# Optimization experiments

Measured on AMD Instinct MI355X. Metric: run time of the kernel, lower is better.

## Reference

```python
import jax, jax.numpy as jnp
import numpy as np

N, B, L = 1000, 16, 12
H, IN_DIM, OUT_DIM, E = 64, 3, 1, 16000


def _gru_cell(x, h, Wi, Wh, bi, bh):
    # torch nn.GRU gate order: r, z, n
    gi = x @ Wi.T + bi
    gh = h @ Wh.T + bh
    ir, iz, inn = jnp.split(gi, 3, axis=-1)
    hr, hz, hn = jnp.split(gh, 3, axis=-1)
    r = jax.nn.sigmoid(ir + hr)
    z = jax.nn.sigmoid(iz + hz)
    n = jnp.tanh(inn + r * hn)
    return (1.0 - z) * n + z * h


def setup_inputs():
    key = jax.random.key(0)
    ks = jax.random.split(key, 24)
    def rn(k, shape, s=0.1):
        return jax.random.normal(k, shape, dtype=jnp.float32) * s
    return {
        "hidden0": rn(ks[0], (N, B, H), 1.0),
        "hidden1": rn(ks[1], (N, B, H), 1.0),
        "features": rn(ks[2], (N, H), 1.0),
        "labels": rn(ks[3], (N, B, L, IN_DIM), 1.0),
        "edge_index": jax.random.randint(ks[4], (2, E), 0, N),
        # GRU1: input_dim -> H
        "Wi1": rn(ks[5], (3 * H, IN_DIM)), "Wh1": rn(ks[6], (3 * H, H)),
        "bi1": rn(ks[7], (3 * H,)), "bh1": rn(ks[8], (3 * H,)),
        # MetaGAT MLP: 2H -> 16 -> 2 -> 2H*H
        "W1": rn(ks[9], (16, 2 * H)), "b1": rn(ks[10], (16,)),
        "W2": rn(ks[11], (2, 16)), "b2": rn(ks[12], (2,)),
        "W3": rn(ks[13], (2 * H * H, 2)), "b3": rn(ks[14], (2 * H * H,)),
        # GRU2: H -> H
        "Wi2": rn(ks[15], (3 * H, H)), "Wh2": rn(ks[16], (3 * H, H)),
        "bi2": rn(ks[17], (3 * H,)), "bh2": rn(ks[18], (3 * H,)),
        # output layer: 2H -> OUT_DIM
        "Wo": rn(ks[19], (OUT_DIM, 2 * H)), "bo": rn(ks[20], (OUT_DIM,)),
    }


def reference(hidden0, hidden1, features, labels, edge_index,
              Wi1, Wh1, bi1, bh1, W1, b1, W2, b2, W3, b3,
              Wi2, Wh2, bi2, bh2, Wo, bo):
    n, b, length, _ = labels.shape
    h = Wh1.shape[1]
    out_dim = Wo.shape[0]
    in_dim = Wi1.shape[1]
    aux = labels[..., out_dim:]  # [N,B,L,aux_dim]
    # add self loops (as in MetaGAT.forward)
    loops = jnp.arange(n)
    src = jnp.concatenate([edge_index[0], loops])  # j, source
    dst = jnp.concatenate([edge_index[1], loops])  # i, target
    # per-edge weight matrices; features are constant across timesteps so hoist
    ft = jnp.concatenate([features[dst], features[src]], axis=-1)  # [Etot,2H]
    w = jax.nn.sigmoid(ft @ W1.T + b1)
    w = jax.nn.sigmoid(w @ W2.T + b2)
    w = (w @ W3.T + b3).reshape(-1, 2 * h, h)  # [Etot,2H,H]
    feat_b = jnp.broadcast_to(features[:, None, :], (n, b, features.shape[-1]))

    def step(carry, idx):
        h0, h1, prev = carry
        aux_prev = jnp.take(aux, jnp.maximum(idx - 1, 0), axis=2)  # [N,B,aux]
        # eval path (train_mode=False): feed back previous prediction
        data = jnp.where(idx == 0,
                         jnp.zeros((n, b, in_dim), labels.dtype),
                         jnp.concatenate([prev, aux_prev], axis=-1))
        h0n = _gru_cell(data.reshape(n * b, in_dim), h0.reshape(n * b, h),
                        Wi1, Wh1, bi1, bh1).reshape(n, b, h)
        # MetaGAT message passing
        st_j = h0n[src]                                  # [Etot,B,H]
        st = jnp.concatenate([h0n[dst], st_j], axis=-1)  # [Etot,B,2H]
        alpha = jax.nn.leaky_relu(jnp.einsum('ebk,ekh->ebh', st, w), 0.01)
        alpha = jax.nn.softmax(alpha, axis=1)            # softmax over batch dim (faithful to source)
        agg = jax.ops.segment_sum(alpha * st_j, dst, num_segments=n)
        gat = jax.nn.relu(agg)                           # [N,B,H]
        h1n = _gru_cell(gat.reshape(n * b, h), h1.reshape(n * b, h),
                        Wi2, Wh2, bi2, bh2).reshape(n, b, h)
        pred = jnp.concatenate([h1n, feat_b], axis=-1) @ Wo.T + bo  # [N,B,out_dim]
        return (h0n, h1n, pred), pred

    init = (hidden0, hidden1, jnp.zeros((n, b, out_dim), labels.dtype))
    _, preds = jax.lax.scan(step, init, jnp.arange(length))
    return jnp.moveaxis(preds, 0, 2)  # [N,B,L,out_dim]
```

## Files before the change

kernel.cpp:

```cpp
#include <hip/hip_runtime.h>

#define N_NODES 1000
#define BATCH 16
#define SEQ 12
#define IN_DIM 3
#define HDIM 64
#define E_EDGES 16000
#define EN (E_EDGES + N_NODES)
#define NB (N_NODES * BATCH)

typedef unsigned int u32;
typedef unsigned short u16;
typedef __fp16 h2_t __attribute__((ext_vector_type(2)));
typedef float f2_t __attribute__((ext_vector_type(2)));

__device__ __forceinline__ float sigmoidf(float x) { return 1.0f / (1.0f + expf(-x)); }

__device__ __forceinline__ u16 f2bf(float x) {
    u32 u = __builtin_bit_cast(u32, x);
    u32 r = (u + 0x7fffu + ((u >> 16) & 1u)) >> 16;
    return (u16)r;
}
__device__ __forceinline__ float bf2f(u32 h) {
    return __builtin_bit_cast(float, (h & 0xffffu) << 16);
}
__device__ __forceinline__ u32 pack2(float a, float b) {
    return (u32)f2bf(a) | ((u32)f2bf(b) << 16);
}

__device__ __forceinline__ u32 pkh2(float a, float b) {
    h2_t h = __builtin_amdgcn_cvt_pkrtz(a, b);
    return __builtin_bit_cast(u32, h);
}
#if __has_builtin(__builtin_amdgcn_fdot2)
__device__ __forceinline__ float dot2(u32 a, u32 b, float c) {
    return __builtin_amdgcn_fdot2(__builtin_bit_cast(h2_t, a),
                                  __builtin_bit_cast(h2_t, b), c, false);
}
#else
__device__ __forceinline__ float dot2(u32 a, u32 b, float c) {
    h2_t x = __builtin_bit_cast(h2_t, a);
    h2_t y = __builtin_bit_cast(h2_t, b);
    return c + (float)x.x * (float)y.x + (float)x.y * (float)y.y;
}
#endif

#if __has_builtin(__builtin_amdgcn_cvt_pk_f32_fp8)
__device__ __forceinline__ f2_t pkf8lo(u32 v) { return __builtin_amdgcn_cvt_pk_f32_fp8(v, false); }
__device__ __forceinline__ f2_t pkf8hi(u32 v) { return __builtin_amdgcn_cvt_pk_f32_fp8(v, true); }
#else
__device__ __forceinline__ f2_t pkf8lo(u32 v) {
    f2_t r; r.x = __builtin_amdgcn_cvt_f32_fp8(v, 0); r.y = __builtin_amdgcn_cvt_f32_fp8(v, 1); return r;
}
__device__ __forceinline__ f2_t pkf8hi(u32 v) {
    f2_t r; r.x = __builtin_amdgcn_cvt_f32_fp8(v, 2); r.y = __builtin_amdgcn_cvt_f32_fp8(v, 3); return r;
}
#endif

__global__ void prep_kernel(const float* __restrict__ hidden0,
                            const float* __restrict__ hidden1,
                            const float* __restrict__ features,
                            const float* __restrict__ W3,
                            const float* __restrict__ b3,
                            const float* __restrict__ Wo,
                            const float* __restrict__ bo,
                            const float* __restrict__ Wh1,
                            const float* __restrict__ Wi1,
                            const float* __restrict__ Wi2,
                            const float* __restrict__ Wh2,
                            float* __restrict__ h0, float* __restrict__ h1,
                            float* __restrict__ M,
                            float* __restrict__ Wh1T, float* __restrict__ Wi1T,
                            u32* __restrict__ W2H2,
                            float* __restrict__ fpred, float* __restrict__ prev)
{
    int tid = blockIdx.x * blockDim.x + threadIdx.x;
    int stride = gridDim.x * blockDim.x;

    for (int i = tid; i < NB * HDIM; i += stride) { h0[i] = hidden0[i]; h1[i] = hidden1[i]; }

    for (int i = tid; i < 64 * 384; i += stride) {
        int k = i / 384, c = i % 384;
        int grp = c / 64, h = c % 64;
        int kk = (grp < 3 ? k : 64 + k) * 64 + h;
        float val;
        if (grp == 0 || grp == 3)      val = W3[kk * 2 + 0];
        else if (grp == 1 || grp == 4) val = W3[kk * 2 + 1];
        else                           val = b3[kk];
        M[i] = val;
    }

    for (int i = tid; i < 192 * 64; i += stride) {
        int k = i / 192, gj = i % 192;
        Wh1T[i] = Wh1[gj * 64 + k];
    }
    for (int i = tid; i < 3 * 192; i += stride) {
        int c = i / 192, gj = i % 192;
        Wi1T[i] = Wi1[gj * 3 + c];
    }

    for (int i = tid; i < 32 * 384; i += stride) {
        int k2 = i / 384, cc = i % 384;
        float v0, v1;
        if (cc < 192) {
            v0 = Wi2[cc * 64 + 2 * k2]; v1 = Wi2[cc * 64 + 2 * k2 + 1];
        } else {
            int gj = cc - 192;
            v0 = Wh2[gj * 64 + 2 * k2]; v1 = Wh2[gj * 64 + 2 * k2 + 1];
        }
        W2H2[i] = pkh2(v0, v1);
    }

    for (int i = tid; i < NB; i += stride) prev[i] = 0.0f;

    for (int n = tid; n < N_NODES; n += stride) {
        float acc = bo[0];
        for (int h = 0; h < HDIM; ++h) acc += features[n * HDIM + h] * Wo[64 + h];
        fpred[n] = acc;
    }
}

__global__ void deg_init_kernel(int* __restrict__ deg)
{
    int n = blockIdx.x * blockDim.x + threadIdx.x;
    if (n < N_NODES) deg[n] = 1;
}

__global__ void deg_count_kernel(const int* __restrict__ edge_index, int* __restrict__ deg)
{
    int e = blockIdx.x * blockDim.x + threadIdx.x;
    if (e < E_EDGES) atomicAdd(&deg[edge_index[E_EDGES + e]], 1);
}

__global__ __launch_bounds__(1024) void scan_kernel(const int* __restrict__ deg,
                                                    int* __restrict__ row_ptr,
                                                    int* __restrict__ row_fill)
{
    __shared__ int s[1024];
    int tid = threadIdx.x;
    int x = (tid < N_NODES) ? deg[tid] : 0;
    s[tid] = x;
    __syncthreads();
    for (int off = 1; off < 1024; off <<= 1) {
        int v = (tid >= off) ? s[tid - off] : 0;
        __syncthreads();
        s[tid] += v;
        __syncthreads();
    }
    int incl = s[tid];
    int excl = incl - x;
    if (tid < N_NODES) { row_ptr[tid] = excl; row_fill[tid] = excl; }
    if (tid == N_NODES - 1) row_ptr[N_NODES] = incl;
}

__global__ void scatter_kernel(const int* __restrict__ edge_index,
                               int* __restrict__ row_fill,
                               int* __restrict__ csr_src,
                               int* __restrict__ perm)
{
    int e = blockIdx.x * blockDim.x + threadIdx.x;
    if (e < E_EDGES) {
        int s = edge_index[e];
        int d = edge_index[E_EDGES + e];
        int p = atomicAdd(&row_fill[d], 1);
        csr_src[p] = s;
        perm[e] = p;
    } else if (e < EN) {
        int n = e - E_EDGES;
        int p = atomicAdd(&row_fill[n], 1);
        csr_src[p] = n;
        perm[e] = p;
    }
}

__global__ __launch_bounds__(256) void edge_mlp_kernel(const int* __restrict__ edge_index,
                                                       const float* __restrict__ features,
                                                       const float* __restrict__ W1,
                                                       const float* __restrict__ b1,
                                                       const float* __restrict__ W2,
                                                       const float* __restrict__ b2,
                                                       const int* __restrict__ perm,
                                                       float* __restrict__ csr_uv)
{
    int w = threadIdx.x >> 6, j = threadIdx.x & 63;
    int e = blockIdx.x * 4 + w;
    int s, d;
    if (e < E_EDGES) { s = edge_index[e]; d = edge_index[E_EDGES + e]; }
    else             { s = e - E_EDGES; d = s; }

    __shared__ float ft[4][128];
    __shared__ float w1s[4][16];
    ft[w][j]      = features[d * HDIM + j];
    ft[w][64 + j] = features[s * HDIM + j];
    __syncthreads();

    int o = j & 15, part = j >> 4;
    float acc = 0.0f;
    #pragma unroll 8
    for (int kk = 0; kk < 32; ++kk)
        acc += ft[w][part * 32 + kk] * W1[o * 128 + part * 32 + kk];
    acc += __shfl_xor(acc, 16, 64);
    acc += __shfl_xor(acc, 32, 64);
    if (j < 16) w1s[w][j] = sigmoidf(acc + b1[j]);
    __syncthreads();
    if (j < 2) {
        float a2 = b2[j];
        #pragma unroll
        for (int k = 0; k < 16; ++k) a2 += w1s[w][k] * W2[j * 16 + k];
        csr_uv[perm[e] * 2 + j] = sigmoidf(a2);
    }
}

__global__ __launch_bounds__(256) void gru1_proj_kernel(const float* __restrict__ labels,
                                                        const float* __restrict__ prev,
                                                        const float* __restrict__ Wi1T,
                                                        const float* __restrict__ Wh1T,
                                                        const float* __restrict__ bi1,
                                                        const float* __restrict__ bh1,
                                                        const float* __restrict__ M,
                                                        float* __restrict__ h0,
                                                        uint2* __restrict__ Pd,
                                                        u32* __restrict__ PsF8,
                                                        int t)
{
    int w = threadIdx.x >> 6, j = threadIdx.x & 63;
    int rbase = blockIdx.x * 32 + w * 8;
    __shared__ float hs[32][64];

    #pragma unroll
    for (int rr = 0; rr < 8; ++rr)
        hs[w * 8 + rr][j] = h0[(size_t)(rbase + rr) * HDIM + j];

    float ar[8], az[8], an[8];
    {
        float br = bh1[j], bz = bh1[64 + j], bn = bh1[128 + j];
        #pragma unroll
        for (int rr = 0; rr < 8; ++rr) { ar[rr] = br; az[rr] = bz; an[rr] = bn; }
    }

    for (int k = 0; k < 64; k += 2) {
        const float* w0 = &Wh1T[(size_t)k * 192 + j];
        float wr0 = w0[0], wz0 = w0[64], wn0 = w0[128];
        float wr1 = w0[192], wz1 = w0[256], wn1 = w0[320];
        #pragma unroll
        for (int rr = 0; rr < 8; ++rr) {
            float2 h2 = *(const float2*)&hs[w * 8 + rr][k];
            ar[rr] = fmaf(wr0, h2.x, ar[rr]);
            az[rr] = fmaf(wz0, h2.x, az[rr]);
            an[rr] = fmaf(wn0, h2.x, an[rr]);
            ar[rr] = fmaf(wr1, h2.y, ar[rr]);
            az[rr] = fmaf(wz1, h2.y, az[rr]);
            an[rr] = fmaf(wn1, h2.y, an[rr]);
        }
    }

    float wi00 = Wi1T[j],       wi01 = Wi1T[64 + j],       wi02 = Wi1T[128 + j];
    float wi10 = Wi1T[192 + j], wi11 = Wi1T[192 + 64 + j], wi12 = Wi1T[192 + 128 + j];
    float wi20 = Wi1T[384 + j], wi21 = Wi1T[384 + 64 + j], wi22 = Wi1T[384 + 128 + j];
    float bir = bi1[j], biz = bi1[64 + j], bin_ = bi1[128 + j];

    #pragma unroll
    for (int rr = 0; rr < 8; ++rr) {
        int row = rbase + rr;
        float x0 = 0.f, x1 = 0.f, x2 = 0.f;
        if (t > 0) {
            x0 = prev[row];
            const float* lab = labels + ((size_t)row * SEQ + (t - 1)) * IN_DIM;
            x1 = lab[1]; x2 = lab[2];
        }
        float gir = bir  + x0 * wi00 + x1 * wi10 + x2 * wi20;
        float giz = biz  + x0 * wi01 + x1 * wi11 + x2 * wi21;
        float gin = bin_ + x0 * wi02 + x1 * wi12 + x2 * wi22;
        float rg = sigmoidf(gir + ar[rr]);
        float zg = sigmoidf(giz + az[rr]);
        float ng = tanhf(gin + rg * an[rr]);
        float hj = hs[w * 8 + rr][j];
        float hn = (1.0f - zg) * ng + zg * hj;
        h0[(size_t)row * HDIM + j] = hn;
        hs[w * 8 + rr][j] = hn;
    }

    float a0[8], a1[8], a2[8], a3[8], a4[8], a5[8];
    #pragma unroll
    for (int rr = 0; rr < 8; ++rr) { a0[rr]=0.f; a1[rr]=0.f; a2[rr]=0.f; a3[rr]=0.f; a4[rr]=0.f; a5[rr]=0.f; }

    for (int k = 0; k < 64; ++k) {
        const float* mrow = &M[(size_t)k * 384 + j];
        float m0 = mrow[0],   m1 = mrow[64],  m2 = mrow[128];
        float m3 = mrow[192], m4 = mrow[256], m5 = mrow[320];
        #pragma unroll
        for (int rr = 0; rr < 8; ++rr) {
            float hk = hs[w * 8 + rr][k];
            a0[rr] = fmaf(m0, hk, a0[rr]); a1[rr] = fmaf(m1, hk, a1[rr]);
            a2[rr] = fmaf(m2, hk, a2[rr]); a3[rr] = fmaf(m3, hk, a3[rr]);
            a4[rr] = fmaf(m4, hk, a4[rr]); a5[rr] = fmaf(m5, hk, a5[rr]);
        }
    }

    #pragma unroll
    for (int rr = 0; rr < 8; ++rr) {
        size_t row = rbase + rr;
        float stj = hs[w * 8 + rr][j];
        Pd[row * 64 + j] = make_uint2(pack2(a0[rr], a1[rr]), pack2(a2[rr], 0.f));
        u32 pk = __builtin_amdgcn_cvt_pk_fp8_f32(a3[rr], a4[rr], 0u, false);
        pk = __builtin_amdgcn_cvt_pk_fp8_f32(a5[rr], stj, pk, true);
        PsF8[row * 64 + j] = pk;
    }
}

__global__ __launch_bounds__(256) void edge_gru2_kernel(const int* __restrict__ row_ptr,
                                                        const int* __restrict__ csr_src,
                                                        const float* __restrict__ csr_uv,
                                                        const uint2* __restrict__ Pd,
                                                        const u32* __restrict__ PsF8,
                                                        const u32* __restrict__ W2H2,
                                                        const float* __restrict__ bi2,
                                                        const float* __restrict__ bh2,
                                                        const float* __restrict__ Wo,
                                                        const float* __restrict__ fpred,
                                                        float* __restrict__ h1,
                                                        float* __restrict__ prev,
                                                        float* __restrict__ out,
                                                        int t)
{
    int d = blockIdx.x;
    int tid = threadIdx.x;
    int w = tid >> 6, j = tid & 63;

    __shared__ float red[4][BATCH][HDIM];
    __shared__ float gs[BATCH][HDIM];
    __shared__ float hs[BATCH][HDIM];
    __shared__ u32 gs2[BATCH][32];
    __shared__ u32 hs2[BATCH][32];

    #pragma unroll
    for (int rr = 0; rr < 4; ++rr)
        hs[w * 4 + rr][j] = h1[(size_t)(d * BATCH + w * 4 + rr) * HDIM + j];

    float pdc0[BATCH], pdc1[BATCH], pdc2[BATCH];
    #pragma unroll
    for (int b = 0; b < BATCH; ++b) {
        uint2 pd = Pd[((size_t)d * BATCH + b) * 64 + j];
        pdc0[b] = bf2f(pd.x);
        pdc1[b] = bf2f(pd.x >> 16);
        pdc2[b] = bf2f(pd.y);
    }

    float acc[BATCH];
    #pragma unroll
    for (int b = 0; b < BATCH; ++b) acc[b] = 0.0f;

    int start = row_ptr[d], end = row_ptr[d + 1];
    for (int p = start + w; p < end; p += 4) {
        int s = csr_src[p];
        float u = csr_uv[p * 2], v = csr_uv[p * 2 + 1];

        float al[BATCH], stj[BATCH];
        #pragma unroll
        for (int b = 0; b < BATCH; ++b) {
            u32 ps = PsF8[((size_t)s * BATCH + b) * 64 + j];
            f2_t lo = pkf8lo(ps);
            f2_t hi = pkf8hi(ps);
            float a = u * (pdc0[b] + lo.x)
                    + v * (pdc1[b] + lo.y)
                    + pdc2[b] + hi.x;
            al[b] = (a > 0.0f) ? a : 0.01f * a;
            stj[b] = hi.y;
        }
        float m = al[0];
        #pragma unroll
        for (int b = 1; b < BATCH; ++b) m = fmaxf(m, al[b]);
        float sum = 0.0f;
        #pragma unroll
        for (int b = 0; b < BATCH; ++b) { al[b] = expf(al[b] - m); sum += al[b]; }
        float inv = 1.0f / sum;
        #pragma unroll
        for (int b = 0; b < BATCH; ++b) acc[b] = fmaf(al[b] * inv, stj[b], acc[b]);
    }

    #pragma unroll
    for (int b = 0; b < BATCH; ++b) red[w][b][j] = acc[b];
    __syncthreads();

    for (int c = tid; c < BATCH * HDIM; c += 256) {
        float s4 = red[0][0][c] + red[1][0][c] + red[2][0][c] + red[3][0][c];
        gs[0][c] = fmaxf(s4, 0.0f);
    }
    __syncthreads();

    for (int q = tid; q < BATCH * 32; q += 256) {
        int r = q >> 5, k2 = q & 31;
        float2 g2v = *(const float2*)&gs[r][k2 * 2];
        gs2[r][k2] = pkh2(g2v.x, g2v.y);
        float2 h2v = *(const float2*)&hs[r][k2 * 2];
        hs2[r][k2] = pkh2(h2v.x, h2v.y);
    }
    __syncthreads();

    float acr[4], acz[4], ain[4], ahn[4];
    {
        float b0 = bi2[j] + bh2[j], b1 = bi2[64 + j] + bh2[64 + j];
        float b2 = bi2[128 + j], c2 = bh2[128 + j];
        #pragma unroll
        for (int rr = 0; rr < 4; ++rr) { acr[rr] = b0; acz[rr] = b1; ain[rr] = b2; ahn[rr] = c2; }
    }

    for (int k2 = 0; k2 < 32; ++k2) {
        u32 wir = W2H2[k2 * 384 + j];
        u32 wiz = W2H2[k2 * 384 + 64 + j];
        u32 win = W2H2[k2 * 384 + 128 + j];
        u32 whr = W2H2[k2 * 384 + 192 + j];
        u32 whz = W2H2[k2 * 384 + 256 + j];
        u32 whn = W2H2[k2 * 384 + 320 + j];
        #pragma unroll
        for (int rr = 0; rr < 4; ++rr) {
            u32 gg = gs2[w * 4 + rr][k2];
            u32 hh = hs2[w * 4 + rr][k2];
            acr[rr] = dot2(wir, gg, acr[rr]);  acr[rr] = dot2(whr, hh, acr[rr]);
            acz[rr] = dot2(wiz, gg, acz[rr]);  acz[rr] = dot2(whz, hh, acz[rr]);
            ain[rr] = dot2(win, gg, ain[rr]);  ahn[rr] = dot2(whn, hh, ahn[rr]);
        }
    }

    float woj = Wo[j];
    float fp = fpred[d];
    #pragma unroll
    for (int rr = 0; rr < 4; ++rr) {
        int row = d * BATCH + w * 4 + rr;
        float rg = sigmoidf(acr[rr]);
        float zg = sigmoidf(acz[rr]);
        float ng = tanhf(ain[rr] + rg * ahn[rr]);
        float hj = hs[w * 4 + rr][j];
        float hn = (1.0f - zg) * ng + zg * hj;
        h1[(size_t)row * HDIM + j] = hn;

        float part = hn * woj;
        #pragma unroll
        for (int off = 32; off; off >>= 1) part += __shfl_xor(part, off, 64);
        if (j == rr) {
            float p = part + fp;
            prev[row] = p;
            out[(size_t)row * SEQ + t] = p;
        }
    }
}

extern "C" void kernel_launch(void* const* d_in, const int* in_sizes, int n_in,
                              void* d_out, int out_size, void* d_ws, size_t ws_size,
                              hipStream_t stream)
{
    const float* hidden0  = (const float*)d_in[0];
    const float* hidden1  = (const float*)d_in[1];
    const float* features = (const float*)d_in[2];
    const float* labels   = (const float*)d_in[3];
    const int*   edge_idx = (const int*)d_in[4];
    const float* Wi1 = (const float*)d_in[5];
    const float* Wh1 = (const float*)d_in[6];
    const float* bi1 = (const float*)d_in[7];
    const float* bh1 = (const float*)d_in[8];
    const float* W1  = (const float*)d_in[9];
    const float* b1  = (const float*)d_in[10];
    const float* W2  = (const float*)d_in[11];
    const float* b2  = (const float*)d_in[12];
    const float* W3  = (const float*)d_in[13];
    const float* b3  = (const float*)d_in[14];
    const float* Wi2 = (const float*)d_in[15];
    const float* Wh2 = (const float*)d_in[16];
    const float* bi2 = (const float*)d_in[17];
    const float* bh2 = (const float*)d_in[18];
    const float* Wo  = (const float*)d_in[19];
    const float* bo  = (const float*)d_in[20];

    float* ws = (float*)d_ws;
    float* h0    = ws;  ws += NB * HDIM;
    float* h1    = ws;  ws += NB * HDIM;
    uint2* Pd    = (uint2*)ws;  ws += NB * HDIM * 2;
    u32*   PsF8  = (u32*)ws;    ws += NB * HDIM;
    float* csr_uv= ws;  ws += EN * 2;
    float* M     = ws;  ws += 64 * 384;
    float* Wh1T  = ws;  ws += 64 * 192;
    float* Wi1T  = ws;  ws += 3 * 192;
    u32*   W2H2  = (u32*)ws;    ws += 32 * 384;
    float* fpred = ws;  ws += N_NODES;
    float* prev  = ws;  ws += NB;
    int*   deg      = (int*)ws;  ws += N_NODES;
    int*   row_ptr  = (int*)ws;  ws += N_NODES + 1;
    int*   row_fill = (int*)ws;  ws += N_NODES;
    int*   csr_src  = (int*)ws;  ws += EN;
    int*   perm     = (int*)ws;  ws += EN;
    float* out   = (float*)d_out;

    prep_kernel<<<256, 256, 0, stream>>>(hidden0, hidden1, features, W3, b3, Wo, bo,
                                         Wh1, Wi1, Wi2, Wh2,
                                         h0, h1, M, Wh1T, Wi1T, W2H2, fpred, prev);
    deg_init_kernel<<<(N_NODES + 255) / 256, 256, 0, stream>>>(deg);
    deg_count_kernel<<<(E_EDGES + 255) / 256, 256, 0, stream>>>(edge_idx, deg);
    scan_kernel<<<1, 1024, 0, stream>>>(deg, row_ptr, row_fill);
    scatter_kernel<<<(EN + 255) / 256, 256, 0, stream>>>(edge_idx, row_fill, csr_src, perm);
    edge_mlp_kernel<<<(EN + 3) / 4, 256, 0, stream>>>(edge_idx, features, W1, b1, W2, b2,
                                                      perm, csr_uv);

    for (int t = 0; t < SEQ; ++t) {
        gru1_proj_kernel<<<NB / 32, 256, 0, stream>>>(labels, prev, Wi1T, Wh1T, bi1, bh1,
                                                      M, h0, Pd, PsF8, t);
        edge_gru2_kernel<<<N_NODES, 256, 0, stream>>>(row_ptr, csr_src, csr_uv, Pd, PsF8,
                                                      W2H2, bi2, bh2, Wo, fpred,
                                                      h1, prev, out, t);
    }
}
```

Before: 849.4 us.

## Fuse next-step GRU1 and projection into edge/GRU2 step kernel with double buffering

Merges the per-timestep GRU1 and projection kernel into the tail of the edge-aggregation/GRU2 kernel, so each timestep needs one launch instead of two. A separate t=0 kernel handles the first step. Pd/Ps buffers are double-buffered so step t reads one copy while writing the next step's projections to the other, and prev is kept in shared memory. GRU1's hidden matmul and the M projection now use packed fp16 dot2 weights instead of fp32 FMAs, which adds precision risk, and launch_bounds(256,4) may limit registers.

```diff
diff --git a/kernel.cpp b/kernel.cpp
--- a/kernel.cpp
+++ b/kernel.cpp
@@ -71,8 +71,9 @@
                             float* __restrict__ h0, float* __restrict__ h1,
                             float* __restrict__ M,
                             float* __restrict__ Wh1T, float* __restrict__ Wi1T,
+                            u32* __restrict__ WhH2, u32* __restrict__ MH2,
                             u32* __restrict__ W2H2,
-                            float* __restrict__ fpred, float* __restrict__ prev)
+                            float* __restrict__ fpred)
 {
     int tid = blockIdx.x * blockDim.x + threadIdx.x;
     int stride = gridDim.x * blockDim.x;
@@ -99,6 +100,28 @@
         Wi1T[i] = Wi1[gj * 3 + c];
     }
 
+    for (int i = tid; i < 32 * 192; i += stride) {
+        int k2 = i / 192, gj = i % 192;
+        WhH2[i] = pkh2(Wh1[gj * 64 + 2 * k2], Wh1[gj * 64 + 2 * k2 + 1]);
+    }
+    for (int i = tid; i < 32 * 384; i += stride) {
+        int k2 = i / 384, c = i % 384;
+        int grp = c / 64, h = c % 64;
+        float v0, v1;
+        {
+            int k = 2 * k2;
+            int kk = (grp < 3 ? k : 64 + k) * 64 + h;
+            v0 = (grp == 0 || grp == 3) ? W3[kk * 2]
+               : (grp == 1 || grp == 4) ? W3[kk * 2 + 1] : b3[kk];
+        }
+        {
+            int k = 2 * k2 + 1;
+            int kk = (grp < 3 ? k : 64 + k) * 64 + h;
+            v1 = (grp == 0 || grp == 3) ? W3[kk * 2]
+               : (grp == 1 || grp == 4) ? W3[kk * 2 + 1] : b3[kk];
+        }
+        MH2[i] = pkh2(v0, v1);
+    }
     for (int i = tid; i < 32 * 384; i += stride) {
         int k2 = i / 384, cc = i % 384;
         float v0, v1;
@@ -110,8 +133,6 @@
         }
         W2H2[i] = pkh2(v0, v1);
     }
-
-    for (int i = tid; i < NB; i += stride) prev[i] = 0.0f;
 
     for (int n = tid; n < N_NODES; n += stride) {
         float acc = bo[0];
@@ -211,17 +232,13 @@
     }
 }
 
-__global__ __launch_bounds__(256) void gru1_proj_kernel(const float* __restrict__ labels,
-                                                        const float* __restrict__ prev,
-                                                        const float* __restrict__ Wi1T,
-                                                        const float* __restrict__ Wh1T,
-                                                        const float* __restrict__ bi1,
-                                                        const float* __restrict__ bh1,
-                                                        const float* __restrict__ M,
-                                                        float* __restrict__ h0,
-                                                        uint2* __restrict__ Pd,
-                                                        u32* __restrict__ PsF8,
-                                                        int t)
+__global__ __launch_bounds__(256) void gru1_proj_t0_kernel(const float* __restrict__ Wh1T,
+                                                           const float* __restrict__ bi1,
+                                                           const float* __restrict__ bh1,
+                                                           const float* __restrict__ M,
+                                                           float* __restrict__ h0,
+                                                           uint2* __restrict__ Pd,
+                                                           u32* __restrict__ PsF8)
 {
     int w = threadIdx.x >> 6, j = threadIdx.x & 63;
     int rbase = blockIdx.x * 32 + w * 8;
@@ -254,29 +271,16 @@
         }
     }
 
-    float wi00 = Wi1T[j],       wi01 = Wi1T[64 + j],       wi02 = Wi1T[128 + j];
-    float wi10 = Wi1T[192 + j], wi11 = Wi1T[192 + 64 + j], wi12 = Wi1T[192 + 128 + j];
-    float wi20 = Wi1T[384 + j], wi21 = Wi1T[384 + 64 + j], wi22 = Wi1T[384 + 128 + j];
     float bir = bi1[j], biz = bi1[64 + j], bin_ = bi1[128 + j];
 
     #pragma unroll
     for (int rr = 0; rr < 8; ++rr) {
-        int row = rbase + rr;
-        float x0 = 0.f, x1 = 0.f, x2 = 0.f;
-        if (t > 0) {
-            x0 = prev[row];
-            const float* lab = labels + ((size_t)row * SEQ + (t - 1)) * IN_DIM;
-            x1 = lab[1]; x2 = lab[2];
-        }
-        float gir = bir  + x0 * wi00 + x1 * wi10 + x2 * wi20;
-        float giz = biz  + x0 * wi01 + x1 * wi11 + x2 * wi21;
-        float gin = bin_ + x0 * wi02 + x1 * wi12 + x2 * wi22;
-        float rg = sigmoidf(gir + ar[rr]);
-        float zg = sigmoidf(giz + az[rr]);
-        float ng = tanhf(gin + rg * an[rr]);
+        float rg = sigmoidf(bir + ar[rr]);
+        float zg = sigmoidf(biz + az[rr]);
+        float ng = tanhf(bin_ + rg * an[rr]);
         float hj = hs[w * 8 + rr][j];
         float hn = (1.0f - zg) * ng + zg * hj;
-        h0[(size_t)row * HDIM + j] = hn;
+        h0[(size_t)(rbase + rr) * HDIM + j] = hn;
         hs[w * 8 + rr][j] = hn;
     }
 
@@ -308,78 +312,91 @@
     }
 }
 
-__global__ __launch_bounds__(256) void edge_gru2_kernel(const int* __restrict__ row_ptr,
-                                                        const int* __restrict__ csr_src,
-                                                        const float* __restrict__ csr_uv,
-                                                        const uint2* __restrict__ Pd,
-                                                        const u32* __restrict__ PsF8,
-                                                        const u32* __restrict__ W2H2,
-                                                        const float* __restrict__ bi2,
-                                                        const float* __restrict__ bh2,
-                                                        const float* __restrict__ Wo,
-                                                        const float* __restrict__ fpred,
-                                                        float* __restrict__ h1,
-                                                        float* __restrict__ prev,
-                                                        float* __restrict__ out,
-                                                        int t)
+__global__ __launch_bounds__(256, 4) void step_kernel(const int* __restrict__ row_ptr,
+                                                      const int* __restrict__ csr_src,
+                                                      const float* __restrict__ csr_uv,
+                                                      const uint2* __restrict__ PdR,
+                                                      const u32* __restrict__ PsR,
+                                                      uint2* __restrict__ PdW,
+                                                      u32* __restrict__ PsW,
+                                                      const u32* __restrict__ W2H2,
+                                                      const float* __restrict__ bi2,
+                                                      const float* __restrict__ bh2,
+                                                      const float* __restrict__ Wo,
+                                                      const float* __restrict__ fpred,
+                                                      float* __restrict__ h1,
+                                                      float* __restrict__ out,
+                                                      const float* __restrict__ labels,
+                                                      const float* __restrict__ Wi1T,
+                                                      const u32* __restrict__ WhH2,
+                                                      const float* __restrict__ bi1,
+                                                      const float* __restrict__ bh1,
+                                                      const u32* __restrict__ MH2,
+                                                      float* __restrict__ h0,
+                                                      int t, int last)
 {
     int d = blockIdx.x;
     int tid = threadIdx.x;
     int w = tid >> 6, j = tid & 63;
+    int rb = w * 4;
+    int growbase = d * BATCH;
 
     __shared__ float red[4][BATCH][HDIM];
     __shared__ float gs[BATCH][HDIM];
-    __shared__ float hs[BATCH][HDIM];
+    __shared__ float hsx[BATCH][HDIM];
     __shared__ u32 gs2[BATCH][32];
     __shared__ u32 hs2[BATCH][32];
+    __shared__ float prevs[BATCH];
 
     #pragma unroll
     for (int rr = 0; rr < 4; ++rr)
-        hs[w * 4 + rr][j] = h1[(size_t)(d * BATCH + w * 4 + rr) * HDIM + j];
-
-    float pdc0[BATCH], pdc1[BATCH], pdc2[BATCH];
-    #pragma unroll
-    for (int b = 0; b < BATCH; ++b) {
-        uint2 pd = Pd[((size_t)d * BATCH + b) * 64 + j];
-        pdc0[b] = bf2f(pd.x);
-        pdc1[b] = bf2f(pd.x >> 16);
-        pdc2[b] = bf2f(pd.y);
-    }
-
-    float acc[BATCH];
-    #pragma unroll
-    for (int b = 0; b < BATCH; ++b) acc[b] = 0.0f;
-
-    int start = row_ptr[d], end = row_ptr[d + 1];
-    for (int p = start + w; p < end; p += 4) {
-        int s = csr_src[p];
-        float u = csr_uv[p * 2], v = csr_uv[p * 2 + 1];
-
-        float al[BATCH], stj[BATCH];
+        hsx[rb + rr][j] = h1[(size_t)(growbase + rb + rr) * HDIM + j];
+
+    {
+        float pdc0[BATCH], pdc1[BATCH], pdc2[BATCH];
         #pragma unroll
         for (int b = 0; b < BATCH; ++b) {
-            u32 ps = PsF8[((size_t)s * BATCH + b) * 64 + j];
-            f2_t lo = pkf8lo(ps);
-            f2_t hi = pkf8hi(ps);
-            float a = u * (pdc0[b] + lo.x)
-                    + v * (pdc1[b] + lo.y)
-                    + pdc2[b] + hi.x;
-            al[b] = (a > 0.0f) ? a : 0.01f * a;
-            stj[b] = hi.y;
-        }
-        float m = al[0];
-        #pragma unroll
-        for (int b = 1; b < BATCH; ++b) m = fmaxf(m, al[b]);
-        float sum = 0.0f;
-        #pragma unroll
-        for (int b = 0; b < BATCH; ++b) { al[b] = expf(al[b] - m); sum += al[b]; }
-        float inv = 1.0f / sum;
-        #pragma unroll
-        for (int b = 0; b < BATCH; ++b) acc[b] = fmaf(al[b] * inv, stj[b], acc[b]);
-    }
-
-    #pragma unroll
-    for (int b = 0; b < BATCH; ++b) red[w][b][j] = acc[b];
+            uint2 pd = PdR[((size_t)growbase + b) * 64 + j];
+            pdc0[b] = bf2f(pd.x);
+            pdc1[b] = bf2f(pd.x >> 16);
+            pdc2[b] = bf2f(pd.y);
+        }
+
+        float acc[BATCH];
+        #pragma unroll
+        for (int b = 0; b < BATCH; ++b) acc[b] = 0.0f;
+
+        int start = row_ptr[d], end = row_ptr[d + 1];
+        for (int p = start + w; p < end; p += 4) {
+            int s = csr_src[p];
+            float u = csr_uv[p * 2], v = csr_uv[p * 2 + 1];
+
+            float al[BATCH], stj[BATCH];
+            #pragma unroll
+            for (int b = 0; b < BATCH; ++b) {
+                u32 ps = PsR[((size_t)s * BATCH + b) * 64 + j];
+                f2_t lo = pkf8lo(ps);
+                f2_t hi = pkf8hi(ps);
+                float a = u * (pdc0[b] + lo.x)
+                        + v * (pdc1[b] + lo.y)
+                        + pdc2[b] + hi.x;
+                al[b] = (a > 0.0f) ? a : 0.01f * a;
+                stj[b] = hi.y;
+            }
+            float m = al[0];
+            #pragma unroll
+            for (int b = 1; b < BATCH; ++b) m = fmaxf(m, al[b]);
+            float sum = 0.0f;
+            #pragma unroll
+            for (int b = 0; b < BATCH; ++b) { al[b] = expf(al[b] - m); sum += al[b]; }
+            float inv = 1.0f / sum;
+            #pragma unroll
+            for (int b = 0; b < BATCH; ++b) acc[b] = fmaf(al[b] * inv, stj[b], acc[b]);
+        }
+
+        #pragma unroll
+        for (int b = 0; b < BATCH; ++b) red[w][b][j] = acc[b];
+    }
     __syncthreads();
 
     for (int c = tid; c < BATCH * HDIM; c += 256) {
@@ -392,55 +409,159 @@
         int r = q >> 5, k2 = q & 31;
         float2 g2v = *(const float2*)&gs[r][k2 * 2];
         gs2[r][k2] = pkh2(g2v.x, g2v.y);
-        float2 h2v = *(const float2*)&hs[r][k2 * 2];
+        float2 h2v = *(const float2*)&hsx[r][k2 * 2];
         hs2[r][k2] = pkh2(h2v.x, h2v.y);
     }
     __syncthreads();
 
-    float acr[4], acz[4], ain[4], ahn[4];
     {
-        float b0 = bi2[j] + bh2[j], b1 = bi2[64 + j] + bh2[64 + j];
-        float b2 = bi2[128 + j], c2 = bh2[128 + j];
-        #pragma unroll
-        for (int rr = 0; rr < 4; ++rr) { acr[rr] = b0; acz[rr] = b1; ain[rr] = b2; ahn[rr] = c2; }
-    }
-
-    for (int k2 = 0; k2 < 32; ++k2) {
-        u32 wir = W2H2[k2 * 384 + j];
-        u32 wiz = W2H2[k2 * 384 + 64 + j];
-        u32 win = W2H2[k2 * 384 + 128 + j];
-        u32 whr = W2H2[k2 * 384 + 192 + j];
-        u32 whz = W2H2[k2 * 384 + 256 + j];
-        u32 whn = W2H2[k2 * 384 + 320 + j];
+        float acr[4], acz[4], ain[4], ahn[4];
+        {
+            float b0 = bi2[j] + bh2[j], b1 = bi2[64 + j] + bh2[64 + j];
+            float b2 = bi2[128 + j], c2 = bh2[128 + j];
+            #pragma unroll
+            for (int rr = 0; rr < 4; ++rr) { acr[rr] = b0; acz[rr] = b1; ain[rr] = b2; ahn[rr] = c2; }
+        }
+
+        for (int k2 = 0; k2 < 32; ++k2) {
+            u32 wir = W2H2[k2 * 384 + j];
+            u32 wiz = W2H2[k2 * 384 + 64 + j];
+            u32 win = W2H2[k2 * 384 + 128 + j];
+            u32 whr = W2H2[k2 * 384 + 192 + j];
+            u32 whz = W2H2[k2 * 384 + 256 + j];
+            u32 whn = W2H2[k2 * 384 + 320 + j];
+            #pragma unroll
+            for (int rr = 0; rr < 4; ++rr) {
+                u32 gg = gs2[rb + rr][k2];
+                u32 hh = hs2[rb + rr][k2];
+                acr[rr] = dot2(wir, gg, acr[rr]);  acr[rr] = dot2(whr, hh, acr[rr]);
+                acz[rr] = dot2(wiz, gg, acz[rr]);  acz[rr] = dot2(whz, hh, acz[rr]);
+                ain[rr] = dot2(win, gg, ain[rr]);  ahn[rr] = dot2(whn, hh, ahn[rr]);
+            }
+        }
+
+        float woj = Wo[j];
+        float fp = fpred[d];
         #pragma unroll
         for (int rr = 0; rr < 4; ++rr) {
-            u32 gg = gs2[w * 4 + rr][k2];
-            u32 hh = hs2[w * 4 + rr][k2];
-            acr[rr] = dot2(wir, gg, acr[rr]);  acr[rr] = dot2(whr, hh, acr[rr]);
-            acz[rr] = dot2(wiz, gg, acz[rr]);  acz[rr] = dot2(whz, hh, acz[rr]);
-            ain[rr] = dot2(win, gg, ain[rr]);  ahn[rr] = dot2(whn, hh, ahn[rr]);
-        }
-    }
-
-    float woj = Wo[j];
-    float fp = fpred[d];
-    #pragma unroll
-    for (int rr = 0; rr < 4; ++rr) {
-        int row = d * BATCH + w * 4 + rr;
-        float rg = sigmoidf(acr[rr]);
-        float zg = sigmoidf(acz[rr]);
-        float ng = tanhf(ain[rr] + rg * ahn[rr]);
-        float hj = hs[w * 4 + rr][j];
-        float hn = (1.0f - zg) * ng + zg * hj;
-        h1[(size_t)row * HDIM + j] = hn;
-
-        float part = hn * woj;
-        #pragma unroll
-        for (int off = 32; off; off >>= 1) part += __shfl_xor(part, off, 64);
-        if (j == rr) {
-            float p = part + fp;
-            prev[row] = p;
-            out[(size_t)row * SEQ + t] = p;
+            int lrow = rb + rr;
+            float rg = sigmoidf(acr[rr]);
+            float zg = sigmoidf(acz[rr]);
+            float ng = tanhf(ain[rr] + rg * ahn[rr]);
+            float hj = hsx[lrow][j];
+            float hn = (1.0f - zg) * ng + zg * hj;
+            h1[(size_t)(growbase + lrow) * HDIM + j] = hn;
+
+            float part = hn * woj;
+            #pragma unroll
+            for (int off = 32; off; off >>= 1) part += __shfl_xor(part, off, 64);
+            if (j == rr) {
+                float p = part + fp;
+                prevs[lrow] = p;
+                out[(size_t)(growbase + lrow) * SEQ + t] = p;
+            }
+        }
+    }
+
+    if (last) return;
+    __syncthreads();
+
+    {
+        #pragma unroll
+        for (int rr = 0; rr < 4; ++rr)
+            hsx[rb + rr][j] = h0[(size_t)(growbase + rb + rr) * HDIM + j];
+        #pragma unroll
+        for (int q = 0; q < 2; ++q) {
+            int idx = q * 64 + j;
+            int r = idx >> 5, k2 = idx & 31;
+            float2 v = *(const float2*)&hsx[rb + r][k2 * 2];
+            hs2[rb + r][k2] = pkh2(v.x, v.y);
+        }
+
+        float ar[4], az[4], an[4];
+        {
+            float br = bh1[j], bz = bh1[64 + j], bn = bh1[128 + j];
+            #pragma unroll
+            for (int rr = 0; rr < 4; ++rr) { ar[rr] = br; az[rr] = bz; an[rr] = bn; }
+        }
+        for (int k2 = 0; k2 < 32; ++k2) {
+            u32 wr = WhH2[k2 * 192 + j];
+            u32 wz = WhH2[k2 * 192 + 64 + j];
+            u32 wn = WhH2[k2 * 192 + 128 + j];
+            #pragma unroll
+            for (int rr = 0; rr < 4; ++rr) {
+                u32 hh = hs2[rb + rr][k2];
+                ar[rr] = dot2(wr, hh, ar[rr]);
+                az[rr] = dot2(wz, hh, az[rr]);
+                an[rr] = dot2(wn, hh, an[rr]);
+            }
+        }
+
+        float wi00 = Wi1T[j],       wi01 = Wi1T[64 + j],       wi02 = Wi1T[128 + j];
+        float wi10 = Wi1T[192 + j], wi11 = Wi1T[192 + 64 + j], wi12 = Wi1T[192 + 128 + j];
+        float wi20 = Wi1T[384 + j], wi21 = Wi1T[384 + 64 + j], wi22 = Wi1T[384 + 128 + j];
+        float bir = bi1[j], biz = bi1[64 + j], bin_ = bi1[128 + j];
+
+        #pragma unroll
+        for (int rr = 0; rr < 4; ++rr) {
+            int lrow = rb + rr;
+            size_t grow = growbase + lrow;
+            float x0 = prevs[lrow];
+            const float* lab = labels + ((size_t)grow * SEQ + t) * IN_DIM;
+            float x1 = lab[1], x2 = lab[2];
+
+            float gir = bir  + x0 * wi00 + x1 * wi10 + x2 * wi20;
+            float giz = biz  + x0 * wi01 + x1 * wi11 + x2 * wi21;
+            float gin = bin_ + x0 * wi02 + x1 * wi12 + x2 * wi22;
+            float rg = sigmoidf(gir + ar[rr]);
+            float zg = sigmoidf(giz + az[rr]);
+            float ng = tanhf(gin + rg * an[rr]);
+            float hj = hsx[lrow][j];
+            float hn = (1.0f - zg) * ng + zg * hj;
+            h0[grow * HDIM + j] = hn;
+            hsx[lrow][j] = hn;
+        }
+
+        #pragma unroll
+        for (int q = 0; q < 2; ++q) {
+            int idx = q * 64 + j;
+            int r = idx >> 5, k2 = idx & 31;
+            float2 v = *(const float2*)&hsx[rb + r][k2 * 2];
+            hs2[rb + r][k2] = pkh2(v.x, v.y);
+        }
+
+        float a0[4], a1[4], a2[4], a3[4], a4[4], a5[4];
+        #pragma unroll
+        for (int rr = 0; rr < 4; ++rr) { a0[rr]=0.f; a1[rr]=0.f; a2[rr]=0.f; a3[rr]=0.f; a4[rr]=0.f; a5[rr]=0.f; }
+
+        for (int k2 = 0; k2 < 32; ++k2) {
+            u32 m0 = MH2[k2 * 384 + j];
+            u32 m1 = MH2[k2 * 384 + 64 + j];
+            u32 m2 = MH2[k2 * 384 + 128 + j];
+            u32 m3 = MH2[k2 * 384 + 192 + j];
+            u32 m4 = MH2[k2 * 384 + 256 + j];
+            u32 m5 = MH2[k2 * 384 + 320 + j];
+            #pragma unroll
+            for (int rr = 0; rr < 4; ++rr) {
+                u32 hh = hs2[rb + rr][k2];
+                a0[rr] = dot2(m0, hh, a0[rr]);
+                a1[rr] = dot2(m1, hh, a1[rr]);
+                a2[rr] = dot2(m2, hh, a2[rr]);
+                a3[rr] = dot2(m3, hh, a3[rr]);
+                a4[rr] = dot2(m4, hh, a4[rr]);
+                a5[rr] = dot2(m5, hh, a5[rr]);
+            }
+        }
+
+        #pragma unroll
+        for (int rr = 0; rr < 4; ++rr) {
+            int lrow = rb + rr;
+            size_t grow = growbase + lrow;
+            float stj = hsx[lrow][j];
+            PdW[grow * 64 + j] = make_uint2(pack2(a0[rr], a1[rr]), pack2(a2[rr], 0.f));
+            u32 pk = __builtin_amdgcn_cvt_pk_fp8_f32(a3[rr], a4[rr], 0u, false);
+            pk = __builtin_amdgcn_cvt_pk_fp8_f32(a5[rr], stj, pk, true);
+            PsW[grow * 64 + j] = pk;
         }
     }
 }
@@ -474,15 +595,19 @@
     float* ws = (float*)d_ws;
     float* h0    = ws;  ws += NB * HDIM;
     float* h1    = ws;  ws += NB * HDIM;
-    uint2* Pd    = (uint2*)ws;  ws += NB * HDIM * 2;
-    u32*   PsF8  = (u32*)ws;    ws += NB * HDIM;
+    uint2* PdBuf[2]; u32* PsBuf[2];
+    PdBuf[0] = (uint2*)ws;  ws += NB * HDIM * 2;
+    PdBuf[1] = (uint2*)ws;  ws += NB * HDIM * 2;
+    PsBuf[0] = (u32*)ws;    ws += NB * HDIM;
+    PsBuf[1] = (u32*)ws;    ws += NB * HDIM;
     float* csr_uv= ws;  ws += EN * 2;
     float* M     = ws;  ws += 64 * 384;
     float* Wh1T  = ws;  ws += 64 * 192;
     float* Wi1T  = ws;  ws += 3 * 192;
-    u32*   W2H2  = (u32*)ws;    ws += 32 * 384;
+    u32*   WhH2  = (u32*)ws;  ws += 32 * 192;
+    u32*   MH2   = (u32*)ws;  ws += 32 * 384;
+    u32*   W2H2  = (u32*)ws;  ws += 32 * 384;
     float* fpred = ws;  ws += N_NODES;
-    float* prev  = ws;  ws += NB;
     int*   deg      = (int*)ws;  ws += N_NODES;
     int*   row_ptr  = (int*)ws;  ws += N_NODES + 1;
     int*   row_fill = (int*)ws;  ws += N_NODES;
@@ -492,7 +617,7 @@
 
     prep_kernel<<<256, 256, 0, stream>>>(hidden0, hidden1, features, W3, b3, Wo, bo,
                                          Wh1, Wi1, Wi2, Wh2,
-                                         h0, h1, M, Wh1T, Wi1T, W2H2, fpred, prev);
+                                         h0, h1, M, Wh1T, Wi1T, WhH2, MH2, W2H2, fpred);
     deg_init_kernel<<<(N_NODES + 255) / 256, 256, 0, stream>>>(deg);
     deg_count_kernel<<<(E_EDGES + 255) / 256, 256, 0, stream>>>(edge_idx, deg);
     scan_kernel<<<1, 1024, 0, stream>>>(deg, row_ptr, row_fill);
@@ -500,11 +625,16 @@
     edge_mlp_kernel<<<(EN + 3) / 4, 256, 0, stream>>>(edge_idx, features, W1, b1, W2, b2,
                                                       perm, csr_uv);
 
+    gru1_proj_t0_kernel<<<NB / 32, 256, 0, stream>>>(Wh1T, bi1, bh1, M, h0,
+                                                     PdBuf[0], PsBuf[0]);
+
     for (int t = 0; t < SEQ; ++t) {
-        gru1_proj_kernel<<<NB / 32, 256, 0, stream>>>(labels, prev, Wi1T, Wh1T, bi1, bh1,
-                                                      M, h0, Pd, PsF8, t);
-        edge_gru2_kernel<<<N_NODES, 256, 0, stream>>>(row_ptr, csr_src, csr_uv, Pd, PsF8,
-                                                      W2H2, bi2, bh2, Wo, fpred,
-                                                      h1, prev, out, t);
-    }
-}
+        int par = t & 1;
+        step_kernel<<<N_NODES, 256, 0, stream>>>(row_ptr, csr_src, csr_uv,
+                                                 PdBuf[par], PsBuf[par],
+                                                 PdBuf[par ^ 1], PsBuf[par ^ 1],
+                                                 W2H2, bi2, bh2, Wo, fpred, h1, out,
+                                                 labels, Wi1T, WhH2, bi1, bh1, MH2, h0,
+                                                 t, (t == SEQ - 1) ? 1 : 0);
+    }
+}
```

Measured after the change: 1.608 ms. +89.3%, slower.
